# Optimization experiments

Hardware: AMD Instinct MI355X
Metric: run time of the kernel (lower is better)

The kernel has to match this reference:

```python
import jax, jax.numpy as jnp
import numpy as np

DIM = 1024
H = 16
HD = 64

def setup_inputs() -> dict:
    key = jax.random.key(0)
    ks = jax.random.split(key, 5)
    x = jax.random.normal(ks[0], (2, 2048, DIM), dtype=jnp.float32)
    gamma = jnp.ones((DIM,), jnp.float32)
    beta = jnp.zeros((DIM,), jnp.float32)
    w_qkv = jax.random.normal(ks[1], (DIM, 3 * H * HD), dtype=jnp.float32) * (DIM ** -0.5)
    w_out = jax.random.normal(ks[2], (H * HD, DIM), dtype=jnp.float32) * ((H * HD) ** -0.5)
    b_out = jnp.zeros((DIM,), jnp.float32)
    return {"x": x, "gamma": gamma, "beta": beta, "w_qkv": w_qkv, "w_out": w_out, "b_out": b_out}

def reference(x, gamma, beta, w_qkv, w_out, b_out):
    # LayerNorm (pre-norm)
    mu = jnp.mean(x, axis=-1, keepdims=True)
    var = jnp.var(x, axis=-1, keepdims=True)
    xn = (x - mu) * jax.lax.rsqrt(var + 1e-5) * gamma + beta
    # QKV projection (no bias)
    qkv = xn @ w_qkv  # (b, n, 3*h*hd)
    q, k, v = jnp.split(qkv, 3, axis=-1)
    b, n, _ = x.shape
    split = lambda t: t.reshape(b, n, H, HD).transpose(0, 2, 1, 3)  # b h n d
    q, k, v = split(q), split(k), split(v)
    scale = HD ** -0.5
    scores = jnp.einsum('bhqd,bhkd->bhqk', q, k) * scale
    weights = jax.nn.softmax(scores, axis=-1)
    attn = jnp.einsum('bhqk,bhkd->bhqd', weights, v)  # b h n d
    attn = attn.transpose(0, 2, 1, 3).reshape(b, n, H * HD)
    # output projection (dropout is identity in eval)
    return attn @ w_out + b_out
```

## Files before the change

kernel.cpp:

```cpp
#include <hip/hip_runtime.h>
#include <hip/hip_bf16.h>


typedef _Float16 f16x8 __attribute__((ext_vector_type(8)));
typedef _Float16 f16x4 __attribute__((ext_vector_type(4)));
typedef float    f32x4 __attribute__((ext_vector_type(4)));

#define DIM   1024
#define NH    16
#define HD2   64
#define SEQ   2048
#define ROWS  4096
#define QKVN  3072

__device__ __forceinline__ void async_copy16(void* lds, const void* gsrc) {
    __builtin_amdgcn_global_load_lds(
        (const __attribute__((address_space(1))) unsigned int*)gsrc,
        (__attribute__((address_space(3))) unsigned int*)lds, 16, 0, 0);
}

__global__ __launch_bounds__(256) void prologue_kernel(
    const float* __restrict__ x, const float* __restrict__ gamma,
    const float* __restrict__ beta, _Float16* __restrict__ xn,
    const float* __restrict__ w_qkv, _Float16* __restrict__ wqkvT,
    const float* __restrict__ w_out, _Float16* __restrict__ woutT) {
    __shared__ float smem[32 * 33];
    const int bid = blockIdx.x;
    const int t = threadIdx.x;
    if (bid < ROWS) {
        const int row = bid;
        const float4 v = reinterpret_cast<const float4*>(x + (size_t)row * DIM)[t];
        float s1 = v.x + v.y + v.z + v.w;
        float s2 = v.x * v.x + v.y * v.y + v.z * v.z + v.w * v.w;
        for (int off = 32; off; off >>= 1) {
            s1 += __shfl_down(s1, off);
            s2 += __shfl_down(s2, off);
        }
        const int wv = t >> 6, lane = t & 63;
        if (lane == 0) { smem[wv * 2] = s1; smem[wv * 2 + 1] = s2; }
        __syncthreads();
        s1 = smem[0] + smem[2] + smem[4] + smem[6];
        s2 = smem[1] + smem[3] + smem[5] + smem[7];
        const float mu = s1 * (1.0f / DIM);
        const float var = s2 * (1.0f / DIM) - mu * mu;
        const float rstd = rsqrtf(var + 1e-5f);
        const float4 g = reinterpret_cast<const float4*>(gamma)[t];
        const float4 bb = reinterpret_cast<const float4*>(beta)[t];
        f16x4 o;
        o[0] = (_Float16)((v.x - mu) * rstd * g.x + bb.x);
        o[1] = (_Float16)((v.y - mu) * rstd * g.y + bb.y);
        o[2] = (_Float16)((v.z - mu) * rstd * g.z + bb.z);
        o[3] = (_Float16)((v.w - mu) * rstd * g.w + bb.w);
        reinterpret_cast<f16x4*>(xn + (size_t)row * DIM)[t] = o;
        return;
    }
    const float* in;
    _Float16* out;
    int C, bx, by;
    if (bid < ROWS + (QKVN / 32) * (DIM / 32)) {
        const int q = bid - ROWS;
        in = w_qkv; out = wqkvT; C = QKVN;
        bx = q % (QKVN / 32); by = q / (QKVN / 32);
    } else {
        const int q = bid - ROWS - (QKVN / 32) * (DIM / 32);
        in = w_out; out = woutT; C = DIM;
        bx = q % (DIM / 32); by = q / (DIM / 32);
    }
    const int R = DIM;
    const int c0 = bx * 32, r0 = by * 32;
    const int tx = t & 31, ty = t >> 5;
    float (*tile)[33] = reinterpret_cast<float(*)[33]>(smem);
#pragma unroll
    for (int i = 0; i < 4; i++)
        tile[ty + i * 8][tx] = in[(size_t)(r0 + ty + i * 8) * C + c0 + tx];
    __syncthreads();
#pragma unroll
    for (int i = 0; i < 4; i++)
        out[(size_t)(c0 + ty + i * 8) * R + r0 + tx] = (_Float16)tile[tx][ty + i * 8];
}

__global__ __launch_bounds__(256) void gemm_qkv_kernel(
    const _Float16* __restrict__ A, const _Float16* __restrict__ Bt,
    _Float16* __restrict__ qk, _Float16* __restrict__ vT, int K) {
    __shared__ _Float16 Al[2][128 * 32];
    __shared__ _Float16 Bl[2][128 * 32];
    const int t = threadIdx.x, wv = t >> 6, lane = t & 63;
    const int lg = lane >> 4, lr = lane & 15;
    const int wr = wv >> 1, wc = wv & 1;
    const int m0 = blockIdx.y * 128, n0 = blockIdx.x * 128;

    f32x4 acc[4][4] = {};

    const int srow = t >> 2, sk = (t & 3) * 8;
    const _Float16* Ag0 = A + (size_t)(m0 + srow) * K + sk;
    const _Float16* Bg0 = Bt + (size_t)(n0 + srow) * K + sk;

    auto STAGE = [&](int buf, int k0) {
        _Float16* Alw = &Al[buf][wv * 512];
        _Float16* Blw = &Bl[buf][wv * 512];
        async_copy16(Alw,        Ag0 + k0);
        async_copy16(Alw + 2048, Ag0 + (size_t)64 * K + k0);
        async_copy16(Blw,        Bg0 + k0);
        async_copy16(Blw + 2048, Bg0 + (size_t)64 * K + k0);
    };

    STAGE(0, 0);
    asm volatile("s_waitcnt vmcnt(0)" ::: "memory");
    __builtin_amdgcn_s_barrier();
    int cur = 0;
    for (int k0 = 0; k0 < K; k0 += 32) {
        if (k0 + 32 < K) STAGE(cur ^ 1, k0 + 32);
        const _Float16* Ab = &Al[cur][0];
        const _Float16* Bb = &Bl[cur][0];
        f16x8 af[4], bfr[4];
#pragma unroll
        for (int m = 0; m < 4; m++)
            af[m] = *reinterpret_cast<const f16x8*>(&Ab[(wr * 64 + m * 16 + lr) * 32 + lg * 8]);
#pragma unroll
        for (int n = 0; n < 4; n++)
            bfr[n] = *reinterpret_cast<const f16x8*>(&Bb[(wc * 64 + n * 16 + lr) * 32 + lg * 8]);
#pragma unroll
        for (int m = 0; m < 4; m++)
#pragma unroll
            for (int n = 0; n < 4; n++)
                acc[m][n] = __builtin_amdgcn_mfma_f32_16x16x32_f16(af[m], bfr[n], acc[m][n], 0, 0, 0);
        asm volatile("s_waitcnt vmcnt(0)" ::: "memory");
        __builtin_amdgcn_s_barrier();
        cur ^= 1;
    }

    if (n0 < 2 * DIM) {
#pragma unroll
        for (int m = 0; m < 4; m++) {
            const int row = m0 + wr * 64 + m * 16 + lg * 4;
#pragma unroll
            for (int n = 0; n < 4; n++) {
                const int col = n0 + wc * 64 + n * 16 + lr;
#pragma unroll
                for (int jj = 0; jj < 4; jj++)
                    qk[(size_t)(row + jj) * 2048 + col] = (_Float16)acc[m][n][jj];
            }
        }
    } else {
#pragma unroll
        for (int m = 0; m < 4; m++) {
            const int row = m0 + wr * 64 + m * 16 + lg * 4;
            const int b = row >> 11, nn = row & 2047;
#pragma unroll
            for (int n = 0; n < 4; n++) {
                const int vcol = n0 + wc * 64 + n * 16 + lr - 2 * DIM;
                f16x4 pk;
#pragma unroll
                for (int jj = 0; jj < 4; jj++) pk[jj] = (_Float16)acc[m][n][jj];
                *reinterpret_cast<f16x4*>(&vT[(size_t)(b * 1024 + vcol) * SEQ + nn]) = pk;
            }
        }
    }
}

__global__ __launch_bounds__(256) void gemm_out_kernel(
    const _Float16* __restrict__ A, const _Float16* __restrict__ Bt,
    float* __restrict__ C, const float* __restrict__ bias, int N, int K) {
    __shared__ _Float16 Al[2][128 * 32];
    __shared__ _Float16 Bl[2][64 * 32];
    const int t = threadIdx.x, wv = t >> 6, lane = t & 63;
    const int lg = lane >> 4, lr = lane & 15;
    const int wr = wv >> 1, wc = wv & 1;
    const int m0 = blockIdx.y * 128, n0 = blockIdx.x * 64;

    f32x4 acc[4][2] = {};

    const int srow = t >> 2, sk = (t & 3) * 8;
    const _Float16* Ag0 = A + (size_t)(m0 + srow) * K + sk;
    const _Float16* Bg0 = Bt + (size_t)(n0 + srow) * K + sk;

    auto STAGE = [&](int buf, int k0) {
        _Float16* Alw = &Al[buf][wv * 512];
        _Float16* Blw = &Bl[buf][wv * 512];
        async_copy16(Alw,        Ag0 + k0);
        async_copy16(Alw + 2048, Ag0 + (size_t)64 * K + k0);
        async_copy16(Blw,        Bg0 + k0);
    };

    STAGE(0, 0);
    asm volatile("s_waitcnt vmcnt(0)" ::: "memory");
    __builtin_amdgcn_s_barrier();
    int cur = 0;
    for (int k0 = 0; k0 < K; k0 += 32) {
        if (k0 + 32 < K) STAGE(cur ^ 1, k0 + 32);
        const _Float16* Ab = &Al[cur][0];
        const _Float16* Bb = &Bl[cur][0];
        f16x8 af[4], bfr[2];
#pragma unroll
        for (int m = 0; m < 4; m++)
            af[m] = *reinterpret_cast<const f16x8*>(&Ab[(wr * 64 + m * 16 + lr) * 32 + lg * 8]);
#pragma unroll
        for (int n = 0; n < 2; n++)
            bfr[n] = *reinterpret_cast<const f16x8*>(&Bb[(wc * 32 + n * 16 + lr) * 32 + lg * 8]);
#pragma unroll
        for (int m = 0; m < 4; m++)
#pragma unroll
            for (int n = 0; n < 2; n++)
                acc[m][n] = __builtin_amdgcn_mfma_f32_16x16x32_f16(af[m], bfr[n], acc[m][n], 0, 0, 0);
        asm volatile("s_waitcnt vmcnt(0)" ::: "memory");
        __builtin_amdgcn_s_barrier();
        cur ^= 1;
    }

#pragma unroll
    for (int m = 0; m < 4; m++) {
        const int row = m0 + wr * 64 + m * 16 + lg * 4;
#pragma unroll
        for (int n = 0; n < 2; n++) {
            const int col = n0 + wc * 32 + n * 16 + lr;
            const float bo = bias[col];
#pragma unroll
            for (int jj = 0; jj < 4; jj++)
                C[(size_t)(row + jj) * N + col] = acc[m][n][jj] + bo;
        }
    }
}

__global__ __launch_bounds__(256, 2) void attn_fa_kernel(
    const _Float16* __restrict__ qk, const _Float16* __restrict__ vT,
    _Float16* __restrict__ attn) {
    const int id = blockIdx.x;
    const int nid = (id & 7) * 64 + (id >> 3);
    const int bh = nid >> 4, b = bh >> 4, h = bh & 15;
    const int q0 = (nid & 15) * 128;
    const int t = threadIdx.x, wv = t >> 6, lane = t & 63;
    const int lg = lane >> 4, lr = lane & 15;

    __shared__ _Float16 Kl[2][64][72];
    __shared__ _Float16 Vt[2][64][72];

    const _Float16* qb = qk + (size_t)(b * SEQ + q0 + wv * 32 + lr) * 2048 + h * HD2;
    f16x8 qf[2][2];
    qf[0][0] = *reinterpret_cast<const f16x8*>(qb + lg * 8);
    qf[0][1] = *reinterpret_cast<const f16x8*>(qb + 32 + lg * 8);
    qf[1][0] = *reinterpret_cast<const f16x8*>(qb + (size_t)16 * 2048 + lg * 8);
    qf[1][1] = *reinterpret_cast<const f16x8*>(qb + (size_t)16 * 2048 + 32 + lg * 8);
#pragma unroll
    for (int qs = 0; qs < 2; qs++) {
        qf[qs][0] = qf[qs][0] * (_Float16)0.125f;
        qf[qs][1] = qf[qs][1] * (_Float16)0.125f;
    }

    f32x4 o[2][4] = {};
    float mrun[2] = {-INFINITY, -INFINITY}, lrun[2] = {0.f, 0.f};

    const int sr = t >> 3, sc = (t & 7) * 8;
    const _Float16* kbase = qk + (size_t)(b * SEQ + sr) * 2048 + DIM + h * HD2 + sc;
    const _Float16* vbase = vT + (size_t)(bh * HD2 + sr) * SEQ + sc;

    f16x8 rk0 = *reinterpret_cast<const f16x8*>(kbase);
    f16x8 rk1 = *reinterpret_cast<const f16x8*>(kbase + (size_t)32 * 2048);
    f16x8 rv0 = *reinterpret_cast<const f16x8*>(vbase);
    f16x8 rv1 = *reinterpret_cast<const f16x8*>(vbase + (size_t)32 * SEQ);
    *reinterpret_cast<f16x8*>(&Kl[0][sr][sc])      = rk0;
    *reinterpret_cast<f16x8*>(&Kl[0][sr + 32][sc]) = rk1;
    *reinterpret_cast<f16x8*>(&Vt[0][sr][sc])      = rv0;
    *reinterpret_cast<f16x8*>(&Vt[0][sr + 32][sc]) = rv1;
    rk0 = *reinterpret_cast<const f16x8*>(kbase + (size_t)64 * 2048);
    rk1 = *reinterpret_cast<const f16x8*>(kbase + (size_t)96 * 2048);
    rv0 = *reinterpret_cast<const f16x8*>(vbase + 64);
    rv1 = *reinterpret_cast<const f16x8*>(vbase + (size_t)32 * SEQ + 64);
    asm volatile("s_waitcnt lgkmcnt(0)" ::: "memory");
    __builtin_amdgcn_s_barrier();

    int p = 0;
    for (int kv0 = 0; kv0 < SEQ; kv0 += 64, p ^= 1) {
        if (kv0 + 64 < SEQ) {
            *reinterpret_cast<f16x8*>(&Kl[p ^ 1][sr][sc])      = rk0;
            *reinterpret_cast<f16x8*>(&Kl[p ^ 1][sr + 32][sc]) = rk1;
            *reinterpret_cast<f16x8*>(&Vt[p ^ 1][sr][sc])      = rv0;
            *reinterpret_cast<f16x8*>(&Vt[p ^ 1][sr + 32][sc]) = rv1;
            if (kv0 + 128 < SEQ) {
                const _Float16* kp = kbase + (size_t)(kv0 + 128) * 2048;
                const _Float16* vp = vbase + (kv0 + 128);
                rk0 = *reinterpret_cast<const f16x8*>(kp);
                rk1 = *reinterpret_cast<const f16x8*>(kp + (size_t)32 * 2048);
                rv0 = *reinterpret_cast<const f16x8*>(vp);
                rv1 = *reinterpret_cast<const f16x8*>(vp + (size_t)32 * SEQ);
            }
        }

        f32x4 s[2][4];
#pragma unroll
        for (int n = 0; n < 4; n++) {
            f16x8 kf0 = *reinterpret_cast<const f16x8*>(&Kl[p][n * 16 + lr][lg * 8]);
            f16x8 kf1 = *reinterpret_cast<const f16x8*>(&Kl[p][n * 16 + lr][32 + lg * 8]);
            __builtin_amdgcn_s_setprio(1);
#pragma unroll
            for (int qs = 0; qs < 2; qs++) {
                f32x4 z = {0.f, 0.f, 0.f, 0.f};
                z = __builtin_amdgcn_mfma_f32_16x16x32_f16(kf0, qf[qs][0], z, 0, 0, 0);
                z = __builtin_amdgcn_mfma_f32_16x16x32_f16(kf1, qf[qs][1], z, 0, 0, 0);
                s[qs][n] = z;
            }
            __builtin_amdgcn_s_setprio(0);
        }

        f16x8 pa[2][2];
#pragma unroll
        for (int qs = 0; qs < 2; qs++) {
            float m1 = fmaxf(fmaxf(s[qs][0][0], s[qs][0][1]), fmaxf(s[qs][0][2], s[qs][0][3]));
#pragma unroll
            for (int n = 1; n < 4; n++)
                m1 = fmaxf(m1, fmaxf(fmaxf(s[qs][n][0], s[qs][n][1]), fmaxf(s[qs][n][2], s[qs][n][3])));
            m1 = fmaxf(m1, __shfl_xor(m1, 16));
            m1 = fmaxf(m1, __shfl_xor(m1, 32));
            if (!__all(m1 - mrun[qs] <= 8.f)) {
                const float mnew = fmaxf(mrun[qs], m1);
                const float corr = __expf(mrun[qs] - mnew);
                mrun[qs] = mnew;
                lrun[qs] *= corr;
#pragma unroll
                for (int dn = 0; dn < 4; dn++) o[qs][dn] *= corr;
            }
            float rsum = 0.f;
#pragma unroll
            for (int n = 0; n < 4; n++)
#pragma unroll
                for (int jj = 0; jj < 4; jj++) {
                    const float pv = __expf(s[qs][n][jj] - mrun[qs]);
                    s[qs][n][jj] = pv;
                    rsum += pv;
                }
            rsum += __shfl_xor(rsum, 16);
            rsum += __shfl_xor(rsum, 32);
            lrun[qs] += rsum;
#pragma unroll
            for (int m = 0; m < 2; m++) {
                f16x8 pv;
#pragma unroll
                for (int jj = 0; jj < 4; jj++) {
                    pv[jj]     = (_Float16)s[qs][2 * m][jj];
                    pv[4 + jj] = (_Float16)s[qs][2 * m + 1][jj];
                }
                pa[qs][m] = pv;
            }
        }

#pragma unroll
        for (int dn = 0; dn < 4; dn++) {
            const _Float16* vr = &Vt[p][dn * 16 + lr][0];
            f16x4 va0 = *reinterpret_cast<const f16x4*>(vr + lg * 4);
            f16x4 va1 = *reinterpret_cast<const f16x4*>(vr + 16 + lg * 4);
            f16x4 vb0 = *reinterpret_cast<const f16x4*>(vr + 32 + lg * 4);
            f16x4 vb1 = *reinterpret_cast<const f16x4*>(vr + 48 + lg * 4);
            f16x8 vf0, vf1;
#pragma unroll
            for (int j = 0; j < 4; j++) {
                vf0[j] = va0[j]; vf0[4 + j] = va1[j];
                vf1[j] = vb0[j]; vf1[4 + j] = vb1[j];
            }
            __builtin_amdgcn_s_setprio(1);
#pragma unroll
            for (int qs = 0; qs < 2; qs++) {
                o[qs][dn] = __builtin_amdgcn_mfma_f32_16x16x32_f16(vf0, pa[qs][0], o[qs][dn], 0, 0, 0);
                o[qs][dn] = __builtin_amdgcn_mfma_f32_16x16x32_f16(vf1, pa[qs][1], o[qs][dn], 0, 0, 0);
            }
            __builtin_amdgcn_s_setprio(0);
        }
        asm volatile("s_waitcnt lgkmcnt(0)" ::: "memory");
        __builtin_amdgcn_s_barrier();
    }

#pragma unroll
    for (int qs = 0; qs < 2; qs++) {
        const float inv = 1.0f / lrun[qs];
        const size_t orow = (size_t)(b * SEQ + q0 + wv * 32 + qs * 16 + lr);
#pragma unroll
        for (int dn = 0; dn < 4; dn++) {
            f16x4 pk;
#pragma unroll
            for (int jj = 0; jj < 4; jj++) pk[jj] = (_Float16)(o[qs][dn][jj] * inv);
            *reinterpret_cast<f16x4*>(&attn[orow * DIM + h * HD2 + dn * 16 + lg * 4]) = pk;
        }
    }
}

extern "C" void kernel_launch(void* const* d_in, const int* in_sizes, int n_in,
                              void* d_out, int out_size, void* d_ws, size_t ws_size,
                              hipStream_t stream) {
    const float* x     = (const float*)d_in[0];
    const float* gamma = (const float*)d_in[1];
    const float* beta  = (const float*)d_in[2];
    const float* w_qkv = (const float*)d_in[3];
    const float* w_out = (const float*)d_in[4];
    const float* b_out = (const float*)d_in[5];
    float* out = (float*)d_out;

    _Float16* ws    = (_Float16*)d_ws;
    _Float16* xn    = ws;
    _Float16* wqkvT = xn + (size_t)ROWS * DIM;
    _Float16* woutT = wqkvT + (size_t)QKVN * DIM;
    _Float16* qk    = woutT + (size_t)DIM * DIM;
    _Float16* vT    = qk + (size_t)ROWS * 2048;
    _Float16* attnb = xn;

    const int pro_blocks = ROWS + (QKVN / 32) * (DIM / 32) + (DIM / 32) * (DIM / 32);
    prologue_kernel<<<pro_blocks, 256, 0, stream>>>(x, gamma, beta, xn, w_qkv, wqkvT, w_out, woutT);
    gemm_qkv_kernel<<<dim3(QKVN / 128, ROWS / 128), 256, 0, stream>>>(xn, wqkvT, qk, vT, DIM);
    attn_fa_kernel<<<512, 256, 0, stream>>>(qk, vT, attnb);
    gemm_out_kernel<<<dim3(DIM / 64, ROWS / 128), 256, 0, stream>>>(attnb, woutT, out, b_out, DIM, DIM);
}
```

Before: 205.4 us.

## Swizzle GEMM block order for XCD locality, repad attention LDS, tree-reduce softmax

Both GEMMs now launch as 1D grids and remap block ids so consecutive blocks on the same XCD (id&7) cover contiguous tiles, aiming for better L2 reuse of A/B panels. The attention kernel's K/V LDS row padding goes from 72 to 76 halves, changing the bank-conflict pattern. The softmax row max and row sum become vectorised tree reductions instead of serial chains, to shorten dependency latency. The padding change could make 16-byte LDS reads misaligned or introduce new conflicts.

```diff
diff --git a/kernel.cpp b/kernel.cpp
--- a/kernel.cpp
+++ b/kernel.cpp
@@ -87,7 +87,10 @@
     const int t = threadIdx.x, wv = t >> 6, lane = t & 63;
     const int lg = lane >> 4, lr = lane & 15;
     const int wr = wv >> 1, wc = wv & 1;
-    const int m0 = blockIdx.y * 128, n0 = blockIdx.x * 128;
+    const int id = blockIdx.x;
+    const int nid = (id & 7) * 96 + (id >> 3);
+    const int bx = nid / 32, by = nid % 32;
+    const int m0 = by * 128, n0 = bx * 128;
 
     f32x4 acc[4][4] = {};
 
@@ -166,7 +169,10 @@
     const int t = threadIdx.x, wv = t >> 6, lane = t & 63;
     const int lg = lane >> 4, lr = lane & 15;
     const int wr = wv >> 1, wc = wv & 1;
-    const int m0 = blockIdx.y * 128, n0 = blockIdx.x * 64;
+    const int id = blockIdx.x;
+    const int nid = (id & 7) * 64 + (id >> 3);
+    const int bx = nid / 32, by = nid % 32;
+    const int m0 = by * 128, n0 = bx * 64;
 
     f32x4 acc[4][2] = {};
 
@@ -231,8 +237,8 @@
     const int t = threadIdx.x, wv = t >> 6, lane = t & 63;
     const int lg = lane >> 4, lr = lane & 15;
 
-    __shared__ _Float16 Kl[2][64][72];
-    __shared__ _Float16 Vt[2][64][72];
+    __shared__ _Float16 Kl[2][64][76];
+    __shared__ _Float16 Vt[2][64][76];
 
     const _Float16* qb = qk + (size_t)(b * SEQ + q0 + wv * 32 + lr) * 2048 + h * HD2;
     f16x8 qf[2][2];
@@ -304,10 +310,14 @@
         f16x8 pa[2][2];
 #pragma unroll
         for (int qs = 0; qs < 2; qs++) {
-            float m1 = fmaxf(fmaxf(s[qs][0][0], s[qs][0][1]), fmaxf(s[qs][0][2], s[qs][0][3]));
-#pragma unroll
-            for (int n = 1; n < 4; n++)
-                m1 = fmaxf(m1, fmaxf(fmaxf(s[qs][n][0], s[qs][n][1]), fmaxf(s[qs][n][2], s[qs][n][3])));
+            f32x4 m4a = s[qs][0], m4b = s[qs][2];
+#pragma unroll
+            for (int jj = 0; jj < 4; jj++) {
+                m4a[jj] = fmaxf(m4a[jj], s[qs][1][jj]);
+                m4b[jj] = fmaxf(m4b[jj], s[qs][3][jj]);
+            }
+            float m1 = fmaxf(fmaxf(fmaxf(m4a[0], m4b[0]), fmaxf(m4a[1], m4b[1])),
+                             fmaxf(fmaxf(m4a[2], m4b[2]), fmaxf(m4a[3], m4b[3])));
             m1 = fmaxf(m1, __shfl_xor(m1, 16));
             m1 = fmaxf(m1, __shfl_xor(m1, 32));
             if (!__all(m1 - mrun[qs] <= 8.f)) {
@@ -318,15 +328,15 @@
 #pragma unroll
                 for (int dn = 0; dn < 4; dn++) o[qs][dn] *= corr;
             }
-            float rsum = 0.f;
 #pragma unroll
             for (int n = 0; n < 4; n++)
 #pragma unroll
-                for (int jj = 0; jj < 4; jj++) {
-                    const float pv = __expf(s[qs][n][jj] - mrun[qs]);
-                    s[qs][n][jj] = pv;
-                    rsum += pv;
-                }
+                for (int jj = 0; jj < 4; jj++)
+                    s[qs][n][jj] = __expf(s[qs][n][jj] - mrun[qs]);
+            f32x4 a4 = s[qs][0] + s[qs][1];
+            f32x4 b4 = s[qs][2] + s[qs][3];
+            a4 = a4 + b4;
+            float rsum = (a4[0] + a4[1]) + (a4[2] + a4[3]);
             rsum += __shfl_xor(rsum, 16);
             rsum += __shfl_xor(rsum, 32);
             lrun[qs] += rsum;
@@ -402,7 +412,7 @@
 
     const int pro_blocks = ROWS + (QKVN / 32) * (DIM / 32) + (DIM / 32) * (DIM / 32);
     prologue_kernel<<<pro_blocks, 256, 0, stream>>>(x, gamma, beta, xn, w_qkv, wqkvT, w_out, woutT);
-    gemm_qkv_kernel<<<dim3(QKVN / 128, ROWS / 128), 256, 0, stream>>>(xn, wqkvT, qk, vT, DIM);
+    gemm_qkv_kernel<<<768, 256, 0, stream>>>(xn, wqkvT, qk, vT, DIM);
     attn_fa_kernel<<<512, 256, 0, stream>>>(qk, vT, attnb);
-    gemm_out_kernel<<<dim3(DIM / 64, ROWS / 128), 256, 0, stream>>>(attnb, woutT, out, b_out, DIM, DIM);
-}
+    gemm_out_kernel<<<512, 256, 0, stream>>>(attnb, woutT, out, b_out, DIM, DIM);
+}
```

New measurement: 200.8 us. 1.02x faster.
